# Optimization experiments

Hardware: AMD Instinct MI355X
Metric: run time of the kernel (lower is better)

The kernel has to match this reference:

```python
import jax, jax.numpy as jnp
import numpy as np
from jax import lax

A_NUM = 3
STRIDES = (4, 8, 16, 32, 64)
LEVEL_HW = ((128, 208), (64, 104), (32, 52), (16, 26), (8, 13))
IMG_H, IMG_W = 512.0, 832.0
PRE_NMS, POST_NMS, NMS_TH = 6000, 1000, 0.7


def _base_anchors(base_size, ratios=(0.5, 1.0, 2.0), scales=(8.0,)):
    ratios = np.asarray(ratios, np.float64)
    scales = np.asarray(scales, np.float64)
    cx = cy = (base_size - 1) / 2.0
    size = float(base_size) * float(base_size)
    ws = np.round(np.sqrt(size / ratios))
    hs = np.round(ws * ratios)
    ws = (ws[:, None] * scales[None, :]).reshape(-1)
    hs = (hs[:, None] * scales[None, :]).reshape(-1)
    return np.stack([cx - 0.5 * (ws - 1), cy - 0.5 * (hs - 1),
                     cx + 0.5 * (ws - 1), cy + 0.5 * (hs - 1)], axis=1)


def _all_anchors():
    # generate_anchors_global: per-level shifted grids, concatenated, order (h, w, a)
    out = []
    for stride, (h, w) in zip(STRIDES, LEVEL_HW):
        base = _base_anchors(stride)  # [A,4]
        sx = np.arange(w) * stride
        sy = np.arange(h) * stride
        sx, sy = np.meshgrid(sx, sy)
        shifts = np.stack([sx.ravel(), sy.ravel(), sx.ravel(), sy.ravel()], axis=1)
        anc = (shifts[:, None, :] + base[None, :, :]).reshape(-1, 4)  # [H*W*A,4]
        out.append(anc)
    return np.concatenate(out, axis=0).astype(np.float32)

_ANCHORS = _all_anchors()


def _conv(x, w, b, pad):
    y = lax.conv_general_dilated(x, w, (1, 1), [(pad, pad), (pad, pad)],
                                 dimension_numbers=('NCHW', 'OIHW', 'NCHW'))
    return y + b[None, :, None, None]


def _bbox_transform_inv(anchors, deltas):
    w = anchors[:, 2] - anchors[:, 0] + 1.0
    h = anchors[:, 3] - anchors[:, 1] + 1.0
    cx = anchors[:, 0] + 0.5 * w
    cy = anchors[:, 1] + 0.5 * h
    dx, dy, dw, dh = deltas[:, 0], deltas[:, 1], deltas[:, 2], deltas[:, 3]
    pcx = dx * w + cx
    pcy = dy * h + cy
    pw = jnp.exp(dw) * w
    ph = jnp.exp(dh) * h
    return jnp.stack([pcx - 0.5 * pw, pcy - 0.5 * ph,
                      pcx + 0.5 * pw, pcy + 0.5 * ph], axis=1)


def _iou_one_to_many(box, boxes):
    area = (boxes[:, 2] - boxes[:, 0] + 1.0) * (boxes[:, 3] - boxes[:, 1] + 1.0)
    area_b = (box[2] - box[0] + 1.0) * (box[3] - box[1] + 1.0)
    xx1 = jnp.maximum(box[0], boxes[:, 0])
    yy1 = jnp.maximum(box[1], boxes[:, 1])
    xx2 = jnp.minimum(box[2], boxes[:, 2])
    yy2 = jnp.minimum(box[3], boxes[:, 3])
    iw = jnp.maximum(0.0, xx2 - xx1 + 1.0)
    ih = jnp.maximum(0.0, yy2 - yy1 + 1.0)
    inter = iw * ih
    return inter / (area + area_b - inter)


def _nms_fixed(boxes, scores, thresh, max_out):
    # greedy NMS with a fixed number of iterations (jit-friendly)
    def body(s, _):
        i = jnp.argmax(s)
        valid = s[i] > -jnp.inf
        ious = _iou_one_to_many(boxes[i], boxes)
        s2 = jnp.where(ious > thresh, -jnp.inf, s)
        s2 = s2.at[i].set(-jnp.inf)
        return s2, (i, valid)
    _, (idx, valid) = lax.scan(body, scores, None, length=max_out)
    return idx, valid


def _rpn_forward(feats, im_info, rpn_conv_w, rpn_conv_b, rpn_score_w,
                 rpn_score_b, rpn_bbox_w, rpn_bbox_b):
    fg_scores, bbox_deltas = [], []
    for p in feats:
        H, W = p.shape[-2], p.shape[-1]
        f = _conv(p, rpn_conv_w, rpn_conv_b, 1)              # [1,512,H,W]
        cls = _conv(f, rpn_score_w, rpn_score_b, 0)          # [1,2A,H,W]
        # _reshape_layer(.,2) + softmax(dim=1) + _reshape_layer back + permute
        prob = jax.nn.softmax(cls.reshape(1, 2, A_NUM, H, W), axis=1)
        prob = prob.reshape(1, 2 * A_NUM, H, W).transpose(0, 2, 3, 1)  # [1,H,W,2A]
        fg = prob[..., A_NUM:].reshape(-1)                    # fg prob, order (h,w,a)
        bb = _conv(f, rpn_bbox_w, rpn_bbox_b, 0).transpose(0, 2, 3, 1).reshape(-1, 4)
        fg_scores.append(fg)
        bbox_deltas.append(bb)
    scores = jnp.concatenate(fg_scores, axis=0)              # [Ntot]
    deltas = jnp.concatenate(bbox_deltas, axis=0)            # [Ntot,4]
    anchors = jnp.asarray(_ANCHORS)

    proposals = _bbox_transform_inv(anchors, deltas)
    # clip to image
    proposals = jnp.stack([
        jnp.clip(proposals[:, 0], 0.0, im_info[1] - 1.0),
        jnp.clip(proposals[:, 1], 0.0, im_info[0] - 1.0),
        jnp.clip(proposals[:, 2], 0.0, im_info[1] - 1.0),
        jnp.clip(proposals[:, 3], 0.0, im_info[0] - 1.0)], axis=1)

    # pre-NMS top-k by score
    top_scores, order = lax.top_k(scores, PRE_NMS)
    top_boxes = proposals[order]
    keep, valid = _nms_fixed(top_boxes, top_scores, NMS_TH, POST_NMS)
    vmask = valid.astype(top_boxes.dtype)[:, None]
    sel_boxes = top_boxes[keep] * vmask
    sel_scores = top_scores[keep][:, None] * vmask
    rois = jnp.concatenate([jnp.zeros((POST_NMS, 1), sel_boxes.dtype), sel_boxes], axis=1)
    return jnp.concatenate([rois, sel_scores], axis=1)        # [POST_NMS, 6]


def setup_inputs() -> dict:
    key = jax.random.key(0)
    ks = jax.random.split(key, 12)
    chans = 256
    feats = {}
    for i, (name, (h, w)) in enumerate(zip(['p2', 'p3', 'p4', 'p5', 'p6'], LEVEL_HW)):
        feats[name] = jax.random.normal(ks[i], (1, chans, h, w), jnp.float32)
    inp = dict(feats)
    inp['im_info'] = jnp.array([IMG_H, IMG_W, 1.0], jnp.float32)
    inp['rpn_conv_w'] = jax.random.normal(ks[5], (512, chans, 3, 3), jnp.float32) * 0.03
    inp['rpn_conv_b'] = jnp.zeros((512,), jnp.float32)
    inp['rpn_score_w'] = jax.random.normal(ks[6], (2 * A_NUM, 512, 1, 1), jnp.float32) * 0.03
    inp['rpn_score_b'] = jnp.zeros((2 * A_NUM,), jnp.float32)
    inp['rpn_bbox_w'] = jax.random.normal(ks[7], (4 * A_NUM, 512, 1, 1), jnp.float32) * 0.01
    inp['rpn_bbox_b'] = jnp.zeros((4 * A_NUM,), jnp.float32)
    return inp


def reference(p2, p3, p4, p5, p6, im_info, rpn_conv_w, rpn_conv_b,
              rpn_score_w, rpn_score_b, rpn_bbox_w, rpn_bbox_b):
    return _rpn_forward([p2, p3, p4, p5, p6], im_info, rpn_conv_w, rpn_conv_b,
                        rpn_score_w, rpn_score_b, rpn_bbox_w, rpn_bbox_b)
```

## Files before the change

### kernel.cpp

```cpp
#include <hip/hip_runtime.h>
#include <stdint.h>

#define N_ANCH   106392
#define PRE_NMS  6000
#define POST_NMS 1000
#define POOL_CAP 8192
#define NMS_BLKS 94
#define SUP_W    96

static __device__ const int    LV_H[5]      = {128, 64, 32, 16, 8};
static __device__ const int    LV_W[5]      = {208, 104, 52, 26, 13};
static __device__ const int    LV_STRIDE[5] = {4, 8, 16, 32, 64};
static __device__ const int    LV_PIX[5]    = {26624, 6656, 1664, 416, 104};
static __device__ const int    LV_TILE0[6]  = {0, 416, 520, 546, 553, 555};
static __device__ const int    LV_AOFF[6]   = {0, 79872, 99840, 104832, 106080, 106392};
static __device__ const int    GPOFF[6]     = {0, 26624, 33280, 34944, 35360, 35464};
static __device__ const double BASE_ANCH[5][3][4] = {
  {{-22.,-10.,25.,13.},   {-14.,-14.,17.,17.},    {-10.,-22.,13.,25.}},
  {{-40.,-20.,47.,27.},   {-28.,-28.,35.,35.},    {-20.,-44.,27.,51.}},
  {{-84.,-40.,99.,55.},   {-56.,-56.,71.,71.},    {-36.,-80.,51.,95.}},
  {{-164.,-72.,195.,103.},{-112.,-112.,143.,143.},{-76.,-168.,107.,199.}},
  {{-332.,-152.,395.,215.},{-224.,-224.,287.,287.},{-148.,-328.,211.,391.}}
};

__device__ __forceinline__ uint32_t sort32f(float f) {
  uint32_t u = __float_as_uint(f);
  return ((int)u < 0) ? ~u : (u | 0x80000000u);
}
__device__ __forceinline__ uint64_t sort64(double d) {
  uint64_t u = (uint64_t)__double_as_longlong(d);
  return ((long long)u < 0) ? ~u : (u | 0x8000000000000000ull);
}

__device__ __forceinline__ double combf(const float* sw, const float* bw, int c, int j) {
  if (j < 3) return (double)sw[(3 + j) * 512 + c] - (double)sw[j * 512 + c];
  return (double)bw[(j - 3) * 512 + c];
}

__global__ __launch_bounds__(256) void k_weff_part(const float* __restrict__ cw,
                                                   const float* __restrict__ sw,
                                                   const float* __restrict__ bw,
                                                   double* __restrict__ Wpart) {
  int chunk = blockIdx.x / 9;
  int tb = blockIdx.x % 9;
  int t = tb * 256 + threadIdx.x;
  int c0 = chunk * 32;
  double acc[15];
#pragma unroll
  for (int j = 0; j < 15; ++j) acc[j] = 0.0;
#pragma unroll 1
  for (int c = c0; c < c0 + 32; ++c) {
    double v = (double)cw[c * 2304 + t];
#pragma unroll
    for (int j = 0; j < 15; ++j) acc[j] += v * combf(sw, bw, c, j);
  }
  double* o = Wpart + (((size_t)chunk * 2304 + t) << 4);
#pragma unroll
  for (int j = 0; j < 15; ++j) o[j] = acc[j];
  o[15] = 0.0;
}

__global__ __launch_bounds__(256) void k_weff_fin(const double* __restrict__ Wpart,
                                                  const float* __restrict__ cb,
                                                  const float* __restrict__ sb,
                                                  const float* __restrict__ bb,
                                                  const float* __restrict__ sw,
                                                  const float* __restrict__ bw,
                                                  double* __restrict__ Weff,
                                                  double* __restrict__ fb,
                                                  float4* __restrict__ w3,
                                                  float* __restrict__ fb32) {
  if (blockIdx.x == 9) {
    __shared__ double ps[15][16];
    int tid = threadIdx.x;
    if (tid < 240) {
      int j = tid >> 4, part = tid & 15;
      double s = 0.0;
      for (int c = part * 32; c < part * 32 + 32; ++c)
        s += (double)cb[c] * combf(sw, bw, c, j);
      ps[j][part] = s;
    }
    __syncthreads();
    if (tid < 15) {
      double s = 0.0;
#pragma unroll
      for (int part = 0; part < 16; ++part) s += ps[tid][part];
      s += (tid < 3) ? ((double)sb[3 + tid] - (double)sb[tid]) : (double)bb[tid - 3];
      fb[tid] = s;
      if (tid < 3) fb32[tid] = (float)s;
    }
    if (tid == 15) fb32[3] = 0.f;
    return;
  }
  int t = blockIdx.x * 256 + threadIdx.x;
  double acc[15];
#pragma unroll
  for (int j = 0; j < 15; ++j) acc[j] = 0.0;
#pragma unroll 1
  for (int chunk = 0; chunk < 16; ++chunk) {
    const double* p = Wpart + (((size_t)chunk * 2304 + t) << 4);
#pragma unroll
    for (int j = 0; j < 15; ++j) acc[j] += p[j];
  }
  double* o = Weff + ((size_t)t << 4);
#pragma unroll
  for (int j = 0; j < 15; ++j) o[j] = acc[j];
  o[15] = 0.0;
  float4 wf;
  wf.x = (float)acc[0]; wf.y = (float)acc[1]; wf.z = (float)acc[2]; wf.w = 0.f;
  w3[t] = wf;
}

__device__ __forceinline__ void load9(float v[9], const float* __restrict__ ib,
                                      const bool rok[3], const bool cok[3],
                                      const int roff[3]) {
#pragma unroll
  for (int ky = 0; ky < 3; ++ky)
#pragma unroll
    for (int kx = 0; kx < 3; ++kx)
      v[ky * 3 + kx] = (rok[ky] && cok[kx]) ? ib[roff[ky] + kx] : 0.0f;
}

__global__ __launch_bounds__(256) void k_fast(
    const float* __restrict__ p0, const float* __restrict__ p1,
    const float* __restrict__ p2, const float* __restrict__ p3,
    const float* __restrict__ p4,
    const float4* __restrict__ w3, const float* __restrict__ fb32,
    float* __restrict__ logits32, uint32_t* __restrict__ hist) {
  __shared__ float4 w3s[2304];
  __shared__ float red[4][64][3];
  int tid = threadIdx.x, wv = tid >> 6, ln = tid & 63;
  for (int i = tid; i < 2304; i += 256) w3s[i] = w3[i];
  int t = blockIdx.x;
  int L = 0;
  while (L < 4 && t >= LV_TILE0[L + 1]) ++L;
  const float* inL = (L == 0) ? p0 : (L == 1) ? p1 : (L == 2) ? p2 : (L == 3) ? p3 : p4;
  int H = LV_H[L], W = LV_W[L], HW = H * W, PIX = LV_PIX[L];
  int pix = (t - LV_TILE0[L]) * 64 + ln;
  bool valid = pix < PIX;
  if (!valid) pix = PIX - 1;
  int h = pix / W, w = pix % W;
  bool rok[3], cok[3];
  int roff[3];
#pragma unroll
  for (int ky = 0; ky < 3; ++ky) {
    int iy = h + ky - 1;
    rok[ky] = (iy >= 0 && iy < H);
    roff[ky] = iy * W + w - 1;
  }
#pragma unroll
  for (int kx = 0; kx < 3; ++kx) {
    int ix = w + kx - 1;
    cok[kx] = (ix >= 0 && ix < W);
  }
  __syncthreads();
  float a0 = 0.f, a1 = 0.f, a2 = 0.f;
  int ci0 = wv * 64;
  const float* ib = inL + ci0 * HW;
#pragma unroll 1
  for (int ci = ci0; ci < ci0 + 64; ++ci, ib += HW) {
    float v[9];
    load9(v, ib, rok, cok, roff);
    const float4* wr = w3s + ci * 9;
#pragma unroll
    for (int t9 = 0; t9 < 9; ++t9) {
      float4 wt = wr[t9];
      float vv = v[t9];
      a0 += vv * wt.x; a1 += vv * wt.y; a2 += vv * wt.z;
    }
  }
  red[wv][ln][0] = a0; red[wv][ln][1] = a1; red[wv][ln][2] = a2;
  __syncthreads();
  if (wv == 0 && valid) {
    int gbase = LV_AOFF[L] + pix * 3;
#pragma unroll
    for (int a = 0; a < 3; ++a) {
      float f = (red[0][ln][a] + red[1][ln][a]) + (red[2][ln][a] + red[3][ln][a]);
      f += fb32[a];
      logits32[gbase + a] = f;
      atomicAdd(&hist[sort32f(f) >> 16], 1u);
    }
  }
}

__global__ __launch_bounds__(1024) void k_edge(const uint32_t* __restrict__ hist,
                                               uint32_t* __restrict__ cnts) {
  __shared__ uint32_t cs[1024];
  __shared__ uint32_t g_grp, g_suf;
  int t = threadIdx.x, wv = t >> 6, ln = t & 63;
#pragma unroll 4
  for (int r = 0; r < 64; ++r) {
    int g = r * 16 + wv;
    uint32_t x = hist[g * 64 + ln];
#pragma unroll
    for (int off = 32; off > 0; off >>= 1) x += __shfl_down(x, off);
    if (ln == 0) cs[g] = x;
  }
  __syncthreads();
  for (int off = 1; off < 1024; off <<= 1) {
    uint32_t v = cs[t] + ((t + off < 1024) ? cs[t + off] : 0u);
    __syncthreads();
    cs[t] = v;
    __syncthreads();
  }
  uint32_t sufnext = (t < 1023) ? cs[t + 1] : 0u;
  if (cs[t] >= PRE_NMS && sufnext < PRE_NMS) {
    g_grp = (uint32_t)t;
    g_suf = sufnext;
  }
  __syncthreads();
  if (t < 64) {
    uint32_t grp = g_grp, suf = g_suf;
    uint32_t x = hist[grp * 64 + t];
    uint32_t S = x;
#pragma unroll
    for (int off = 1; off < 64; off <<= 1) {
      uint32_t y = __shfl_down(S, off);
      if (t + off < 64) S += y;
    }
    unsigned long long mask = __ballot(suf + S >= PRE_NMS);
    int hi = 63 - (int)__clzll(mask);
    if (t == hi) {
      uint32_t e = grp * 64 + (uint32_t)hi;
      cnts[1] = (e > 2) ? e - 2 : 0;
    }
  }
}

__global__ __launch_bounds__(256) void k_compact(const float* __restrict__ logits32,
                                                 uint32_t* __restrict__ cnts,
                                                 uint32_t* __restrict__ alist) {
  int i = blockIdx.x * 256 + threadIdx.x;
  if (i >= N_ANCH) return;
  if ((sort32f(logits32[i]) >> 16) >= cnts[1]) {
    uint32_t pos = atomicAdd(&cnts[0], 1u);
    if (pos < POOL_CAP) alist[pos] = (uint32_t)i;
  }
}

__global__ __launch_bounds__(256) void k_refine(
    const float* __restrict__ p0, const float* __restrict__ p1,
    const float* __restrict__ p2, const float* __restrict__ p3,
    const float* __restrict__ p4,
    const double* __restrict__ Weff, const double* __restrict__ fb,
    const uint32_t* __restrict__ alist, const uint32_t* __restrict__ cnts,
    double* __restrict__ logits, double* __restrict__ deltas,
    uint64_t* __restrict__ pkey) {
  __shared__ double red[4][64][5];
  int tid = threadIdx.x, wv = tid >> 6, ln = tid & 63;
  int cnt = (int)cnts[0];
  if (cnt > POOL_CAP) cnt = POOL_CAP;
  int base = blockIdx.x * 64;
  if (base >= cnt) return;
  int slot = base + ln;
  if (slot >= cnt) slot = cnt - 1;
  int gi = (int)alist[slot];
  int gpix = gi / 3, a = gi - gpix * 3;
  int L = 0;
  while (L < 4 && gpix >= GPOFF[L + 1]) ++L;
  int pix = gpix - GPOFF[L];
  const float* inL = (L == 0) ? p0 : (L == 1) ? p1 : (L == 2) ? p2 : (L == 3) ? p3 : p4;
  int H = LV_H[L], W = LV_W[L], HW = H * W;
  int h = pix / W, w = pix % W;
  bool rok[3], cok[3];
  int roff[3];
#pragma unroll
  for (int ky = 0; ky < 3; ++ky) {
    int iy = h + ky - 1;
    rok[ky] = (iy >= 0 && iy < H);
    roff[ky] = iy * W + w - 1;
  }
#pragma unroll
  for (int kx = 0; kx < 3; ++kx) {
    int ix = w + kx - 1;
    cok[kx] = (ix >= 0 && ix < W);
  }
  double sc = 0.0, d0 = 0.0, d1 = 0.0, d2 = 0.0, d3 = 0.0;
  int js = a, jd = 3 + 4 * a;
  int ci0 = wv * 64;
  const float* ib = inL + ci0 * HW;
#pragma unroll 1
  for (int ci = ci0; ci < ci0 + 64; ++ci, ib += HW) {
    float v[9];
    load9(v, ib, rok, cok, roff);
    const double* wr = Weff + ((size_t)ci * 144);
#pragma unroll
    for (int t9 = 0; t9 < 9; ++t9) {
      double vd = (double)v[t9];
      const double* wt = wr + t9 * 16;
      sc += vd * wt[js];
      d0 += vd * wt[jd + 0];
      d1 += vd * wt[jd + 1];
      d2 += vd * wt[jd + 2];
      d3 += vd * wt[jd + 3];
    }
  }
  red[wv][ln][0] = sc;
  red[wv][ln][1] = d0; red[wv][ln][2] = d1;
  red[wv][ln][3] = d2; red[wv][ln][4] = d3;
  __syncthreads();
  if (wv == 0) {
    double f[5];
#pragma unroll
    for (int j = 0; j < 5; ++j)
      f[j] = red[0][ln][j] + red[1][ln][j] + red[2][ln][j] + red[3][ln][j];
    double lg = f[0] + fb[js];
    logits[gi] = lg;
    deltas[gi * 4 + 0] = f[1] + fb[jd + 0];
    deltas[gi * 4 + 1] = f[2] + fb[jd + 1];
    deltas[gi * 4 + 2] = f[3] + fb[jd + 2];
    deltas[gi * 4 + 3] = f[4] + fb[jd + 3];
    pkey[slot] = (sort64(lg) & ~0x1FFFFull) | (uint64_t)(0x1FFFFu - (uint32_t)gi);
  }
}

__global__ __launch_bounds__(256) void k_rank_cnt(const uint32_t* __restrict__ cnts,
                                                  const uint64_t* __restrict__ pkey,
                                                  uint32_t* __restrict__ rank32) {
  __shared__ uint64_t lk[512];
  int t = threadIdx.x;
  int cnt = (int)cnts[0];
  if (cnt > POOL_CAP) cnt = POOL_CAP;
  int it = blockIdx.x >> 4, jc = blockIdx.x & 15;
  int e = it * 256 + t;
  int c0 = jc * 512;
  if (it * 256 >= cnt || c0 >= cnt) return;
  int lim = cnt - c0; if (lim > 512) lim = 512;
  for (int i = t; i < 512; i += 256) lk[i] = (i < lim) ? pkey[c0 + i] : 0ull;
  __syncthreads();
  bool active = e < cnt;
  uint64_t mykey = active ? pkey[e] : ~0ull;
  int r = 0;
#pragma unroll 8
  for (int j = 0; j < 512; ++j) r += (lk[j] > mykey) ? 1 : 0;
  if (active && r) atomicAdd(&rank32[e], (uint32_t)r);
}

__global__ __launch_bounds__(256) void k_scatter(const uint32_t* __restrict__ cnts,
                                                 const uint64_t* __restrict__ pkey,
                                                 const uint32_t* __restrict__ rank32,
                                                 const double* __restrict__ logits,
                                                 const double* __restrict__ deltas,
                                                 const float* __restrict__ im_info,
                                                 double* __restrict__ ss,
                                                 double* __restrict__ sbx,
                                                 float4* __restrict__ bxf,
                                                 float* __restrict__ areaf) {
  int t = threadIdx.x;
  int cnt = (int)cnts[0];
  if (cnt > POOL_CAP) cnt = POOL_CAP;
  int e = blockIdx.x * 256 + t;
  if (blockIdx.x * 256 >= cnt) return;
  if (e >= cnt) return;
  int rank = (int)rank32[e];
  if (rank >= PRE_NMS) return;
  uint64_t mykey = pkey[e];
  int gi = 0x1FFFF - (int)(mykey & 0x1FFFFull);
  int L = 0;
  while (L < 4 && gi >= LV_AOFF[L + 1]) ++L;
  int rel = gi - LV_AOFF[L];
  int pix = rel / 3, a = rel % 3;
  int W = LV_W[L];
  int h = pix / W, w = pix % W;
  double imW1 = (double)im_info[1] - 1.0;
  double imH1 = (double)im_info[0] - 1.0;
  double shx = (double)(w * LV_STRIDE[L]), shy = (double)(h * LV_STRIDE[L]);
  double ax1 = BASE_ANCH[L][a][0] + shx, ay1 = BASE_ANCH[L][a][1] + shy;
  double ax2 = BASE_ANCH[L][a][2] + shx, ay2 = BASE_ANCH[L][a][3] + shy;
  double dx = deltas[gi * 4 + 0], dy = deltas[gi * 4 + 1];
  double dw = deltas[gi * 4 + 2], dh = deltas[gi * 4 + 3];
  double wa = ax2 - ax1 + 1.0, ha = ay2 - ay1 + 1.0;
  double cx = ax1 + 0.5 * wa, cy = ay1 + 0.5 * ha;
  double pcx = dx * wa + cx, pcy = dy * ha + cy;
  double pw = exp(dw) * wa, ph = exp(dh) * ha;
  double x1 = fmin(fmax(pcx - 0.5 * pw, 0.0), imW1);
  double y1 = fmin(fmax(pcy - 0.5 * ph, 0.0), imH1);
  double x2 = fmin(fmax(pcx + 0.5 * pw, 0.0), imW1);
  double y2 = fmin(fmax(pcy + 0.5 * ph, 0.0), imH1);
  ss[rank] = 1.0 / (1.0 + exp(-logits[gi]));
  sbx[rank * 4 + 0] = x1; sbx[rank * 4 + 1] = y1;
  sbx[rank * 4 + 2] = x2; sbx[rank * 4 + 3] = y2;
  float4 bf;
  bf.x = (float)x1; bf.y = (float)y1; bf.z = (float)x2; bf.w = (float)y2;
  bxf[rank] = bf;
  areaf[rank] = (float)((x2 - x1 + 1.0) * (y2 - y1 + 1.0));
}

__device__ __forceinline__ bool iou_gt(const double* A, const double* B) {
  double areaA = (A[2] - A[0] + 1.0) * (A[3] - A[1] + 1.0);
  double areaB = (B[2] - B[0] + 1.0) * (B[3] - B[1] + 1.0);
  double xx1 = fmax(A[0], B[0]), yy1 = fmax(A[1], B[1]);
  double xx2 = fmin(A[2], B[2]), yy2 = fmin(A[3], B[3]);
  double iw = fmax(0.0, xx2 - xx1 + 1.0), ih = fmax(0.0, yy2 - yy1 + 1.0);
  double inter = iw * ih;
  return inter > 0.7 * (areaA + areaB - inter);
}

__global__ __launch_bounds__(256) void k_build(const double* __restrict__ sbx,
                                               const float4* __restrict__ bxf,
                                               const float* __restrict__ areaf,
                                               uint64_t* __restrict__ Sup) {
  __shared__ float cbx[256][5];
  __shared__ float rbx[64][5];
  int blk = blockIdx.x;
  int rtile = blk / 24, ctile = blk % 24;
  int t = threadIdx.x, q = t >> 6, ln = t & 63;
  int r = rtile * 64 + ln;
  int w = ctile * 4 + q;
  {
    int c = ctile * 256 + t;
    float4 b;
    float ar;
    if (c < NMS_BLKS * 64) { b = bxf[c]; ar = areaf[c]; }
    else { b.x = b.y = b.z = b.w = 0.f; ar = 0.f; }
    cbx[t][0] = b.x; cbx[t][1] = b.y; cbx[t][2] = b.z; cbx[t][3] = b.w; cbx[t][4] = ar;
    if (t < 64) {
      int rr = rtile * 64 + t;
      float4 rb = bxf[rr];
      rbx[t][0] = rb.x; rbx[t][1] = rb.y; rbx[t][2] = rb.z; rbx[t][3] = rb.w;
      rbx[t][4] = areaf[rr];
    }
  }
  __syncthreads();
  uint64_t bits = 0ull;
  int j0 = w * 64;
  if (w < NMS_BLKS && j0 + 63 > r) {
    float ax1 = rbx[ln][0], ay1 = rbx[ln][1], ax2 = rbx[ln][2], ay2 = rbx[ln][3];
    float aar = rbx[ln][4];
#pragma unroll 4
    for (int jj = 0; jj < 64; ++jj) {
      int j = j0 + jj;
      if (j <= r) continue;
      int cl = q * 64 + jj;
      float iw = fminf(ax2, cbx[cl][2]) - fmaxf(ax1, cbx[cl][0]) + 1.f;
      float ih = fminf(ay2, cbx[cl][3]) - fmaxf(ay1, cbx[cl][1]) + 1.f;
      float inter = fmaxf(iw, 0.f) * fmaxf(ih, 0.f);
      float d = inter - 0.7f * (aar + cbx[cl][4] - inter);
      bool sup;
      if (d > 4.0f) sup = true;
      else if (d < -4.0f) sup = false;
      else sup = iou_gt(sbx + (size_t)r * 4, sbx + (size_t)j * 4);
      if (sup) bits |= 1ull << jj;
    }
  }
  Sup[(size_t)r * SUP_W + w] = bits;
}

__global__ __launch_bounds__(1024) void k_scan(const uint64_t* __restrict__ Sup,
                                               const double* __restrict__ ss,
                                               const double* __restrict__ sbx,
                                               float* __restrict__ out) {
  __shared__ uint16_t keep[POST_NMS];
  __shared__ uint32_t ext_arr[NMS_BLKS][2];
  __shared__ int s_kcnt;
  int t = threadIdx.x, wv = t >> 6, ln = t & 63;
  for (int i = t; i < NMS_BLKS * 2; i += 1024) ext_arr[i >> 1][i & 1] = 0u;
  if (t == 0) s_kcnt = 0;
  uint64_t nrow = 0ull;
  if (wv == 0) nrow = Sup[(size_t)ln * SUP_W];
  __syncthreads();
  for (int b = 0; b < NMS_BLKS; ++b) {
    if (wv == 0) {
      uint64_t myrow = nrow & ~((2ull << ln) - 1ull);
      if (b + 1 < NMS_BLKS)
        nrow = Sup[(size_t)((b + 1) * 64 + ln) * SUP_W + (b + 1)];
      uint64_t ext = ((uint64_t)ext_arr[b][1] << 32) | ext_arr[b][0];
      int base = b * 64;
      if (base + 63 >= PRE_NMS) {
        int v = PRE_NMS - base;
        ext |= ~((1ull << v) - 1ull);
      }
      int K0 = s_kcnt;
      uint64_t avail = ~ext;
      uint64_t kp = 0ull;
      int lim = POST_NMS - K0, nk = 0;
      while (avail && nk < lim) {
        int i2 = __ffsll((unsigned long long)avail) - 1;
        kp |= 1ull << i2;
        ++nk;
        uint64_t row = __shfl(myrow, i2);
        avail &= ~row;
        avail &= ~(1ull << i2);
      }
      if ((kp >> ln) & 1ull) {
        int pos = K0 + __popcll(kp & ((1ull << ln) - 1ull));
        keep[pos] = (uint16_t)(base + ln);
      }
      if (ln == 0) s_kcnt = K0 + nk;
    }
    __syncthreads();
    int K = s_kcnt;
    if (K >= POST_NMS || b + 1 >= NMS_BLKS) break;
    uint64_t m = 0ull;
    for (int p = t; p < K; p += 1024) m |= Sup[(size_t)keep[p] * SUP_W + (b + 1)];
#pragma unroll
    for (int off = 32; off > 0; off >>= 1) m |= __shfl_down(m, off);
    if (ln == 0 && m) {
      uint32_t lo = (uint32_t)m, hi = (uint32_t)(m >> 32);
      if (lo) atomicOr(&ext_arr[b + 1][0], lo);
      if (hi) atomicOr(&ext_arr[b + 1][1], hi);
    }
    __syncthreads();
  }
  __syncthreads();
  int KF = s_kcnt;
  for (int r = t; r < POST_NMS; r += 1024) {
    float* o = out + r * 6;
    if (r < KF) {
      int p = keep[r];
      o[0] = 0.f;
      o[1] = (float)sbx[p * 4 + 0];
      o[2] = (float)sbx[p * 4 + 1];
      o[3] = (float)sbx[p * 4 + 2];
      o[4] = (float)sbx[p * 4 + 3];
      o[5] = (float)ss[p];
    } else {
#pragma unroll
      for (int c = 0; c < 6; ++c) o[c] = 0.f;
    }
  }
}

extern "C" void kernel_launch(void* const* d_in, const int* in_sizes, int n_in,
                              void* d_out, int out_size, void* d_ws, size_t ws_size,
                              hipStream_t stream) {
  const float* p0 = (const float*)d_in[0];
  const float* p1 = (const float*)d_in[1];
  const float* p2 = (const float*)d_in[2];
  const float* p3 = (const float*)d_in[3];
  const float* p4 = (const float*)d_in[4];
  const float* im_info = (const float*)d_in[5];
  const float* cw = (const float*)d_in[6];
  const float* cb = (const float*)d_in[7];
  const float* sw = (const float*)d_in[8];
  const float* sb = (const float*)d_in[9];
  const float* bw = (const float*)d_in[10];
  const float* bb = (const float*)d_in[11];
  char* ws = (char*)d_ws;
  uint32_t* hist    = (uint32_t*)(ws + 0);
  uint32_t* cnts    = (uint32_t*)(ws + 262144);
  double*   fb      = (double*)  (ws + 262208);
  float*    fb32    = (float*)   (ws + 262336);
  double*   logits  = (double*)  (ws + 262352);
  double*   deltas  = (double*)  (ws + 1113488);
  float*    logits32= (float*)   (ws + 4518032);
  float4*   w3      = (float4*)  (ws + 4943600);
  double*   Weff    = (double*)  (ws + 4980464);
  double*   Wpart   = (double*)  (ws + 5275376);
  uint32_t* alist   = (uint32_t*)(ws + 9993968);
  double*   ssort   = (double*)  (ws + 10026736);
  double*   sbx     = (double*)  (ws + 10074864);
  float4*   bxf     = (float4*)  (ws + 10267376);
  float*    areaf   = (float*)   (ws + 10363632);
  uint64_t* Sup     = (uint64_t*)(ws + 10387696);
  uint64_t* pkey    = (uint64_t*)(ws + 15007984);
  uint32_t* rank32  = (uint32_t*)(ws + 15073520);
  float* out = (float*)d_out;

  hipMemsetAsync(ws, 0, 262208, stream);
  hipMemsetAsync(rank32, 0, 32768, stream);
  k_weff_part<<<144, 256, 0, stream>>>(cw, sw, bw, Wpart);
  k_weff_fin<<<10, 256, 0, stream>>>(Wpart, cb, sb, bb, sw, bw, Weff, fb, w3, fb32);
  k_fast<<<555, 256, 0, stream>>>(p0, p1, p2, p3, p4, w3, fb32, logits32, hist);
  k_edge<<<1, 1024, 0, stream>>>(hist, cnts);
  k_compact<<<416, 256, 0, stream>>>(logits32, cnts, alist);
  k_refine<<<128, 256, 0, stream>>>(p0, p1, p2, p3, p4, Weff, fb, alist, cnts,
                                    logits, deltas, pkey);
  k_rank_cnt<<<512, 256, 0, stream>>>(cnts, pkey, rank32);
  k_scatter<<<32, 256, 0, stream>>>(cnts, pkey, rank32, logits, deltas, im_info,
                                    ssort, sbx, bxf, areaf);
  k_build<<<94 * 24, 256, 0, stream>>>(sbx, bxf, areaf, Sup);
  k_scan<<<1, 1024, 0, stream>>>(Sup, ssort, sbx, out);
}
```

Baseline: 489.3 us.

## Make candidate compaction deterministic via block-count prefix sum; batch refine channel loads

Replaces the atomic-append compaction of candidate anchors with a two-pass scheme: one kernel counts passing anchors per block with ballots, a second computes each block's offset by summing earlier block counts and writes indices in anchor order. This gives a stable candidate order and avoids contention on a global atomic, at the cost of an extra launch and a redundant prefix reduction in every block. Separately, the refine kernel now loads four channels' 3x3 windows before accumulating, so more memory loads are in flight per iteration, which uses more registers.

```diff
diff --git a/kernel.cpp b/kernel.cpp
--- a/kernel.cpp
+++ b/kernel.cpp
@@ -227,15 +227,51 @@
   }
 }
 
-__global__ __launch_bounds__(256) void k_compact(const float* __restrict__ logits32,
-                                                 uint32_t* __restrict__ cnts,
-                                                 uint32_t* __restrict__ alist) {
-  int i = blockIdx.x * 256 + threadIdx.x;
-  if (i >= N_ANCH) return;
-  if ((sort32f(logits32[i]) >> 16) >= cnts[1]) {
-    uint32_t pos = atomicAdd(&cnts[0], 1u);
+__global__ __launch_bounds__(256) void k_cnt(const float* __restrict__ logits32,
+                                             const uint32_t* __restrict__ cnts,
+                                             uint32_t* __restrict__ bcnt) {
+  __shared__ uint32_t wc[4];
+  int tid = threadIdx.x;
+  int i = blockIdx.x * 256 + tid;
+  uint32_t edge = cnts[1];
+  bool pass = (i < N_ANCH) && ((sort32f(logits32[i]) >> 16) >= edge);
+  unsigned long long m = __ballot(pass);
+  if ((tid & 63) == 0) wc[tid >> 6] = (uint32_t)__popcll(m);
+  __syncthreads();
+  if (tid == 0) bcnt[blockIdx.x] = wc[0] + wc[1] + wc[2] + wc[3];
+}
+
+__global__ __launch_bounds__(256) void k_fill(const float* __restrict__ logits32,
+                                              uint32_t* __restrict__ cnts,
+                                              const uint32_t* __restrict__ bcnt,
+                                              uint32_t* __restrict__ alist) {
+  __shared__ uint32_t red[256];
+  __shared__ uint32_t woff[4];
+  int tid = threadIdx.x, wv = tid >> 6, ln = tid & 63;
+  uint32_t s = 0;
+  for (int k = tid; k < blockIdx.x; k += 256) s += bcnt[k];
+  red[tid] = s;
+  __syncthreads();
+#pragma unroll
+  for (int off = 128; off > 0; off >>= 1) {
+    if (tid < off) red[tid] += red[tid + off];
+    __syncthreads();
+  }
+  uint32_t base = red[0];
+  int i = blockIdx.x * 256 + tid;
+  uint32_t edge = cnts[1];
+  bool pass = (i < N_ANCH) && ((sort32f(logits32[i]) >> 16) >= edge);
+  unsigned long long m = __ballot(pass);
+  if (ln == 0) woff[wv] = (uint32_t)__popcll(m);
+  __syncthreads();
+  uint32_t off_in_blk = 0;
+  for (int k = 0; k < wv; ++k) off_in_blk += woff[k];
+  if (pass) {
+    uint32_t pos = base + off_in_blk + (uint32_t)__popcll(m & ((1ull << ln) - 1ull));
     if (pos < POOL_CAP) alist[pos] = (uint32_t)i;
   }
+  if (blockIdx.x == ((N_ANCH + 255) / 256 - 1) && tid == 0)
+    cnts[0] = base + woff[0] + woff[1] + woff[2] + woff[3];
 }
 
 __global__ __launch_bounds__(256) void k_refine(
@@ -280,20 +316,28 @@
   int ci0 = wv * 64;
   const float* ib = inL + ci0 * HW;
 #pragma unroll 1
-  for (int ci = ci0; ci < ci0 + 64; ++ci, ib += HW) {
-    float v[9];
-    load9(v, ib, rok, cok, roff);
+  for (int ci = ci0; ci < ci0 + 64; ci += 4) {
+    float v[4][9];
+    {
+      const float* ibb = ib;
+#pragma unroll
+      for (int u = 0; u < 4; ++u, ibb += HW) load9(v[u], ibb, rok, cok, roff);
+    }
     const double* wr = Weff + ((size_t)ci * 144);
 #pragma unroll
-    for (int t9 = 0; t9 < 9; ++t9) {
-      double vd = (double)v[t9];
-      const double* wt = wr + t9 * 16;
-      sc += vd * wt[js];
-      d0 += vd * wt[jd + 0];
-      d1 += vd * wt[jd + 1];
-      d2 += vd * wt[jd + 2];
-      d3 += vd * wt[jd + 3];
-    }
+    for (int u = 0; u < 4; ++u, wr += 144) {
+#pragma unroll
+      for (int t9 = 0; t9 < 9; ++t9) {
+        double vd = (double)v[u][t9];
+        const double* wt = wr + t9 * 16;
+        sc += vd * wt[js];
+        d0 += vd * wt[jd + 0];
+        d1 += vd * wt[jd + 1];
+        d2 += vd * wt[jd + 2];
+        d3 += vd * wt[jd + 3];
+      }
+    }
+    ib += 4 * HW;
   }
   red[wv][ln][0] = sc;
   red[wv][ln][1] = d0; red[wv][ln][2] = d1;
@@ -555,6 +599,7 @@
   uint64_t* Sup     = (uint64_t*)(ws + 10387696);
   uint64_t* pkey    = (uint64_t*)(ws + 15007984);
   uint32_t* rank32  = (uint32_t*)(ws + 15073520);
+  uint32_t* bcnt    = hist;
   float* out = (float*)d_out;
 
   hipMemsetAsync(ws, 0, 262208, stream);
@@ -563,7 +608,8 @@
   k_weff_fin<<<10, 256, 0, stream>>>(Wpart, cb, sb, bb, sw, bw, Weff, fb, w3, fb32);
   k_fast<<<555, 256, 0, stream>>>(p0, p1, p2, p3, p4, w3, fb32, logits32, hist);
   k_edge<<<1, 1024, 0, stream>>>(hist, cnts);
-  k_compact<<<416, 256, 0, stream>>>(logits32, cnts, alist);
+  k_cnt<<<416, 256, 0, stream>>>(logits32, cnts, bcnt);
+  k_fill<<<416, 256, 0, stream>>>(logits32, cnts, bcnt, alist);
   k_refine<<<128, 256, 0, stream>>>(p0, p1, p2, p3, p4, Weff, fb, alist, cnts,
                                     logits, deltas, pkey);
   k_rank_cnt<<<512, 256, 0, stream>>>(cnts, pkey, rank32);
```

Result: slower. 656.2 us (+34.1%).
